# Kernel optimization log

Measured on AMD Instinct MI355X. Metric: run time of the kernel, lower is better.

## Reference

```python
import jax, jax.numpy as jnp
import numpy as np

B, D, MAXC = 16384, 64, 8
NPROB, NCON, TDIM, HID = 50000, 2000, 1024, 256

def setup_inputs() -> dict:
    key = jax.random.key(0)
    ks = jax.random.split(key, 20)
    s = 0.02
    return {
        'prob_ids': jax.random.randint(ks[0], (B,), 0, NPROB),
        'related_concept_index': jax.random.randint(ks[1], (B, MAXC), 0, NCON),
        'filter0': jax.random.randint(ks[2], (B, MAXC), 0, 2),
        'h': jax.random.normal(ks[3], (B, D), jnp.float32),
        'emb': jax.random.normal(ks[4], (B, 2 * D), jnp.float32),
        'operate': jax.random.randint(ks[5], (B, 1), 0, 2).astype(jnp.float32),
        'exercise_text_emb': jax.random.normal(ks[6], (NPROB, TDIM), jnp.float32) * s,
        'concept_text_emb': jax.random.normal(ks[7], (NCON, TDIM), jnp.float32) * s,
        'W1': jax.random.normal(ks[8], (TDIM, HID), jnp.float32) * s,
        'b1': jnp.zeros((HID,), jnp.float32),
        'W2': jax.random.normal(ks[9], (HID, D), jnp.float32) * s,
        'b2': jnp.zeros((D,), jnp.float32),
        'Wp': jax.random.normal(ks[10], (5 * D, 1), jnp.float32) * s,
        'bp': jnp.zeros((1,), jnp.float32),
        'Wx': jax.random.normal(ks[11], (4 * D, 3 * D), jnp.float32) * s,
        'Wh': jax.random.normal(ks[12], (D, 3 * D), jnp.float32) * s,
        'bx': jnp.zeros((3 * D,), jnp.float32),
        'bh': jnp.zeros((3 * D,), jnp.float32),
    }

def reference(prob_ids, related_concept_index, filter0, h, emb, operate,
              exercise_text_emb, concept_text_emb,
              W1, b1, W2, b2, Wp, bp, Wx, Wh, bx, bh):
    def text_proj(x):  # 1024 -> 256 -> 64 (dropout off at inference)
        return jax.nn.relu(x @ W1 + b1) @ W2 + b2

    red_prob = text_proj(exercise_text_emb)      # [NPROB, D]
    red_con = text_proj(concept_text_emb)        # [NCON, D]

    related = red_con[related_concept_index]     # gather: [B, MAXC, D]

    # text weights: cosine similarity of raw BERT embs (torch eps=1e-8)
    q = exercise_text_emb[prob_ids]              # [B, 1024]
    c = concept_text_emb[related_concept_index]  # [B, MAXC, 1024]
    dot = jnp.einsum('bd,bmd->bm', q, c)
    qn = jnp.sqrt(jnp.sum(q * q, axis=-1))[:, None]
    cn = jnp.sqrt(jnp.sum(c * c, axis=-1))
    tw = dot / jnp.maximum(qn * cn, 1e-8)
    tw = jnp.where(filter0 == 0, jnp.float32(-1e9), tw)
    tw = jax.nn.softmax(tw, axis=1)              # [B, MAXC]

    rep = jnp.einsum('bmd,bm->bd', related, tw)  # weighted concept sum
    v = jnp.concatenate([red_prob[prob_ids], rep], axis=1)  # [B, 2D]

    # predictor: funcs(n_layer=1, dim*5, 1) ~ single Linear
    prob = jnp.concatenate([h, v, emb], axis=1) @ Wp + bp   # [B, 1]

    # update_state -> GRU cell (mygru: input 4D, hidden D)
    op = operate
    v_cat = jnp.concatenate([v * op, v * (1 - op)], axis=1)
    e_cat = jnp.concatenate([emb * (1 - op), emb * op], axis=1)
    x = v_cat + e_cat                             # [B, 4D]
    xg = x @ Wx + bx
    hg = h @ Wh + bh
    xr, xz, xn = jnp.split(xg, 3, axis=1)
    hr, hz, hn = jnp.split(hg, 3, axis=1)
    r = jax.nn.sigmoid(xr + hr)
    z = jax.nn.sigmoid(xz + hz)
    n = jnp.tanh(xn + r * hn)
    h_next = (1 - z) * n + z * h                  # [B, D]
    return (prob, h_next)
```

## Files before the change

### kernel.cpp

```cpp
#include <hip/hip_runtime.h>
#include <cstdint>
#include <cstddef>

typedef unsigned short u16;
typedef unsigned char u8;
typedef long long i64;
typedef unsigned long long u64;
typedef __bf16 bf16x8 __attribute__((ext_vector_type(8)));
typedef float f32x4 __attribute__((ext_vector_type(4)));
typedef float f32x2 __attribute__((ext_vector_type(2)));
typedef u16 u16x8 __attribute__((ext_vector_type(8)));

#define B_ 16384
#define D_ 64
#define MAXC_ 8
#define NCON_ 2000
#define NCONP_ 2048
#define TDIM_ 1024
#define HID_ 256

#define VMW(n) asm volatile("s_waitcnt vmcnt(" #n ")" ::: "memory")
#define BAR() __builtin_amdgcn_s_barrier()

__device__ inline u16 f2b(float f){
  unsigned u = __float_as_uint(f);
  u += 0x7fffu + ((u >> 16) & 1u);
  return (u16)(u >> 16);
}
__device__ inline float b2f(u16 u){ return __uint_as_float(((unsigned)u) << 16); }

__device__ inline unsigned pk2fp8(float a, float b){
  return (unsigned)__builtin_amdgcn_cvt_pk_fp8_f32(a, b, 0, false);
}

__device__ inline void gload16(const void* g, void* l){
  __builtin_amdgcn_global_load_lds((const __attribute__((address_space(1))) unsigned*)g,
                                   (__attribute__((address_space(3))) unsigned*)l, 16, 0, 0);
}

__device__ inline float wsum(float v){
  #pragma unroll
  for (int o = 32; o; o >>= 1) v += __shfl_xor(v, o);
  return v;
}
__device__ inline float sigf(float x){ return 1.f / (1.f + __expf(-x)); }

__global__ __launch_bounds__(256) void k_prep(
    const float* __restrict__ ex, const int* __restrict__ pid,
    const float* __restrict__ con,
    const float* __restrict__ W1, const float* __restrict__ W2,
    const float* __restrict__ Wx, const float* __restrict__ Wh,
    const float* __restrict__ bx, const float* __restrict__ bh,
    u8* __restrict__ qb8, float* __restrict__ qn,
    u8* __restrict__ cb8, float* __restrict__ cn,
    u8* __restrict__ W1T8, u16* __restrict__ W2T, u16* __restrict__ WxhT,
    float* __restrict__ bxh)
{
  const int bid = blockIdx.x, tid = threadIdx.x;
  const int lane = tid & 63;
  if (bid < 4096){
    const int b = bid * 4 + (tid >> 6);
    const float* src = ex + (size_t)pid[b] * TDIM_;
    u8* dst8 = qb8 + (size_t)b * TDIM_;
    float ss = 0.f;
    #pragma unroll
    for (int c = 0; c < 4; ++c){
      float4 v = *(const float4*)(src + c * 256 + lane * 4);
      ss += v.x*v.x + v.y*v.y + v.z*v.z + v.w*v.w;
      unsigned lo = pk2fp8(v.x * 32.f, v.y * 32.f);
      unsigned hi = pk2fp8(v.z * 32.f, v.w * 32.f);
      *(unsigned*)(dst8 + c * 256 + lane * 4) = (lo & 0xffffu) | (hi << 16);
    }
    ss = wsum(ss);
    if (lane == 0) qn[b] = sqrtf(ss);
  } else if (bid < 4608){
    const int r = (bid - 4096) * 4 + (tid >> 6);
    u8* dst8 = cb8 + (size_t)r * TDIM_;
    if (r < NCON_){
      const float* src = con + (size_t)r * TDIM_;
      float ss = 0.f;
      #pragma unroll
      for (int c = 0; c < 4; ++c){
        float4 v = *(const float4*)(src + c * 256 + lane * 4);
        ss += v.x*v.x + v.y*v.y + v.z*v.z + v.w*v.w;
        unsigned lo = pk2fp8(v.x * 32.f, v.y * 32.f);
        unsigned hi = pk2fp8(v.z * 32.f, v.w * 32.f);
        *(unsigned*)(dst8 + c * 256 + lane * 4) = (lo & 0xffffu) | (hi << 16);
      }
      ss = wsum(ss);
      if (lane == 0) cn[r] = sqrtf(ss);
    } else {
      #pragma unroll
      for (int c = 0; c < 4; ++c)
        *(unsigned*)(dst8 + c * 256 + lane * 4) = 0u;
    }
  } else {
    int gid = (bid - 4608) * 256 + tid;
    if (gid < 131072){
      int n = gid >> 9, k2 = (gid & 511) * 2;
      unsigned pk = pk2fp8(W1[(size_t)k2 * 256 + n] * 32.f,
                           W1[(size_t)(k2 + 1) * 256 + n] * 32.f);
      *(u16*)(W1T8 + (size_t)n * 1024 + k2) = (u16)pk;
    } else if (gid < 147456){
      int t = gid - 131072;
      int n = t >> 8, k = t & 255;
      W2T[t] = f2b(W2[(size_t)k * 64 + n]);
    } else if (gid < 229376){
      int t = gid - 147456;
      int c = t / 320, k = t % 320;
      int g = (c >> 4) & 3;
      int d = (c >> 6) * 16 + (c & 15);
      float v = 0.f;
      if (k < 256){
        if (g == 0)      v = Wx[(size_t)k * 192 + d];
        else if (g == 1) v = Wx[(size_t)k * 192 + 64 + d];
        else if (g == 2) v = Wx[(size_t)k * 192 + 128 + d];
      } else {
        int kh = k - 256;
        if (g == 0)      v = Wh[(size_t)kh * 192 + d];
        else if (g == 1) v = Wh[(size_t)kh * 192 + 64 + d];
        else if (g == 3) v = Wh[(size_t)kh * 192 + 128 + d];
      }
      WxhT[t] = f2b(v);
    } else if (gid < 229632){
      int c = gid - 229376;
      int g = (c >> 4) & 3;
      int d = (c >> 6) * 16 + (c & 15);
      float v;
      if (g == 0)      v = bx[d] + bh[d];
      else if (g == 1) v = bx[64 + d] + bh[64 + d];
      else if (g == 2) v = bx[128 + d];
      else             v = bh[128 + d];
      bxh[c] = v;
    }
  }
}

__global__ __launch_bounds__(512) void k_mlp(
    const u8* __restrict__ qb8, const u8* __restrict__ cb8,
    const u8* __restrict__ W1T8, const float* __restrict__ b1,
    const u16* __restrict__ W2T, const float* __restrict__ b2,
    float* __restrict__ redq, float* __restrict__ redc)
{
  __shared__ char SMm[53248];
  u16* Hs = (u16*)(SMm + 36864);
  const int tid = threadIdx.x;
  const int lane = tid & 63;
  const int w = tid >> 6;
  const int lr = lane & 15, lq = lane >> 4;
  const bool qside = blockIdx.x < 512;
  const u8* Abase = qside ? qb8 : cb8;
  float* Obase = qside ? redq : redc;
  const int m0 = (qside ? (int)blockIdx.x : ((int)blockIdx.x - 512)) << 5;
  const int rf = w & 1, ch = w >> 1;

  auto stage = [&](int buf, int kt){
    u8* Ab = (u8*)SMm + buf * 18432;
    u8* Bb = Ab + 2048;
    #pragma unroll
    for (int i = 0; i < 2; ++i){
      int e = i * 512 + tid;
      int slot = e >> 2, q4 = e & 3;
      int sw = (slot ^ (slot >> 2)) & 3;
      gload16(W1T8 + (size_t)slot * 1024 + kt * 64 + ((q4 ^ sw) << 4), Bb + e * 16);
    }
    if (tid < 128){
      int slot = tid >> 2, q4 = tid & 3;
      int sw = (slot ^ (slot >> 2)) & 3;
      gload16(Abase + (size_t)(m0 + slot) * TDIM_ + kt * 64 + ((q4 ^ sw) << 4),
              Ab + tid * 16);
    }
  };

  f32x4 acc[4] = {};
  stage(0, 0);
  int buf = 0;
  for (int kt = 0; kt < 16; ++kt){
    if (kt < 15){
      stage(buf ^ 1, kt + 1);
      if (w < 2) VMW(3); else VMW(2);
    } else VMW(0);
    BAR();
    const u8* Ab = (const u8*)SMm + buf * 18432;
    const u8* Bb = Ab + 2048;
    #pragma unroll
    for (int ks = 0; ks < 2; ++ks){
      const int h8 = ks * 4 + lq;
      const int arow = rf * 16 + lr;
      const int asw = (arow ^ (arow >> 2)) & 3;
      i64 a = *(const i64*)(Ab + arow * 64 + (((h8 >> 1) ^ asw) << 4) + (h8 & 1) * 8);
      #pragma unroll
      for (int fc = 0; fc < 4; ++fc){
        int brow = ch * 64 + fc * 16 + lr;
        int bsw = (brow ^ (brow >> 2)) & 3;
        i64 bv = *(const i64*)(Bb + brow * 64 + (((h8 >> 1) ^ bsw) << 4) + (h8 & 1) * 8);
        acc[fc] = __builtin_amdgcn_mfma_f32_16x16x32_fp8_fp8(a, bv, acc[fc], 0, 0, 0);
      }
    }
    BAR();
    buf ^= 1;
  }
  #pragma unroll
  for (int fc = 0; fc < 4; ++fc){
    int col = ch * 64 + fc * 16 + lr;
    float bv = b1[col];
    #pragma unroll
    for (int j = 0; j < 4; ++j){
      int rr = rf * 16 + lq * 4 + j;
      float v = fmaxf(acc[fc][j] * (1.f / 1024.f) + bv, 0.f);
      *(u16*)((char*)Hs + rr * 512 + ((col * 2) ^ ((rr & 7) << 4))) = f2b(v);
    }
  }
  __syncthreads();
  const int rf2 = w & 1, cp = w >> 1;
  f32x4 acc2 = {};
  #pragma unroll
  for (int ks2 = 0; ks2 < 8; ++ks2){
    int rr = rf2 * 16 + lr;
    int kb2 = ks2 * 64 + lq * 16;
    bf16x8 af2 = *(const bf16x8*)((const char*)Hs + rr * 512 + (kb2 ^ ((rr & 7) << 4)));
    bf16x8 w2 = *(const bf16x8*)(W2T + (size_t)(cp * 16 + lr) * 256 + ks2 * 32 + lq * 8);
    acc2 = __builtin_amdgcn_mfma_f32_16x16x32_bf16(af2, w2, acc2, 0, 0, 0);
  }
  {
    int col = cp * 16 + lr;
    float bv = b2[col];
    #pragma unroll
    for (int j = 0; j < 4; ++j){
      int rr = m0 + rf2 * 16 + lq * 4 + j;
      Obase[(size_t)rr * 64 + col] = acc2[j] + bv;
    }
  }
}

__global__ __launch_bounds__(512) void k_mixgru(
    const u8* __restrict__ qb8, const u8* __restrict__ cb8,
    const float* __restrict__ qn, const float* __restrict__ cn,
    const int* __restrict__ rci, const int* __restrict__ filt,
    const float* __restrict__ redq, const float* __restrict__ redc,
    const float* __restrict__ h, const float* __restrict__ emb,
    const float* __restrict__ op, const float* __restrict__ Wp,
    const float* __restrict__ bp, const u16* __restrict__ WxhT,
    const float* __restrict__ bxh, float* __restrict__ prob_out,
    float* __restrict__ outh)
{
  __shared__ char SM[67584];
  u8*    QsF  = (u8*)SM;
  u16*   XH   = (u16*)SM;
  float* DOTS = (float*)(SM + 20480);
  int*   SIDX = (int*)(SM + 32768);
  int*   SFLT = (int*)(SM + 33792);
  u8*    CsB  = (u8*)(SM + 34816);
  u16*   Bs   = (u16*)(SM + 34816);
  const int tid = threadIdx.x;
  const int lane = tid & 63;
  const int w = tid >> 6;
  const int m0 = blockIdx.x << 5;

  auto stageC = [&](int buf, int kt){
    #pragma unroll
    for (int i = 0; i < 2; ++i){
      int e = i * 512 + tid;
      int slot = e >> 2, q4 = e & 3;
      int sw = (slot ^ (slot >> 2)) & 3;
      gload16(cb8 + (size_t)SIDX[slot] * TDIM_ + kt * 64 + ((q4 ^ sw) << 4),
              CsB + buf * 16384 + e * 16);
    }
  };

  if (tid < 256) SIDX[tid] = rci[m0 * MAXC_ + tid];
  else           SFLT[tid - 256] = filt[m0 * MAXC_ + (tid - 256)];
  __syncthreads();
  #pragma unroll
  for (int i = 0; i < 4; ++i){
    int e = i * 512 + tid;
    int row = e >> 6, c16 = e & 63;
    gload16(qb8 + (size_t)(m0 + row) * TDIM_ + ((c16 ^ (row & 7)) << 4),
            QsF + e * 16);
  }
  stageC(0, 0);

  const int R = w >> 2;
  const int cc0 = (w & 3) * 2;
  f32x4 dacc[2] = {};
  int bufc = 0;
  for (int kt = 0; kt < 16; ++kt){
    if (kt < 15){ stageC(bufc ^ 1, kt + 1); VMW(2); }
    else        { VMW(0); }
    BAR();
    const u8* Cs = CsB + bufc * 16384;
    #pragma unroll
    for (int ks = 0; ks < 2; ++ks){
      const int h8 = ks * 4 + (lane >> 4);
      const int arow = R * 16 + (lane & 15);
      const int c16r = kt * 4 + (h8 >> 1);
      i64 a = *(const i64*)(QsF + arow * 1024 + ((c16r ^ (arow & 7)) << 4) + (h8 & 1) * 8);
      #pragma unroll
      for (int t = 0; t < 2; ++t){
        int slot = (R * 8 + cc0 + t) * 16 + (lane & 15);
        int bsw = (slot ^ (slot >> 2)) & 3;
        i64 bfr = *(const i64*)(Cs + slot * 64 + (((h8 >> 1) ^ bsw) << 4) + (h8 & 1) * 8);
        dacc[t] = __builtin_amdgcn_mfma_f32_16x16x32_fp8_fp8(a, bfr, dacc[t], 0, 0, 0);
      }
    }
    BAR();
    bufc ^= 1;
  }
  #pragma unroll
  for (int t = 0; t < 2; ++t){
    const int cc = cc0 + t;
    const int col = lane & 15;
    #pragma unroll
    for (int j = 0; j < 4; ++j){
      int tr = (lane >> 4) * 4 + j;
      if (tr == 2 * cc && col < 8)       DOTS[(R * 16 + tr) * 8 + col] = dacc[t][j];
      if (tr == 2 * cc + 1 && col >= 8)  DOTS[(R * 16 + tr) * 8 + col - 8] = dacc[t][j];
    }
  }
  auto stageB = [&](int kt){
    #pragma unroll
    for (int i = 0; i < 4; ++i){
      int cc = i * 512 + tid;
      int r2 = cc >> 3, s2 = cc & 7;
      gload16(WxhT + (size_t)r2 * 320 + kt * 64 + ((s2 ^ (r2 & 7)) << 3), &Bs[cc * 8]);
    }
  };
  __syncthreads();
  stageB(0);

  for (int i = 0; i < 4; ++i){
    const int r = w * 4 + i;
    const int b = m0 + r;
    int idxm[MAXC_];
    #pragma unroll
    for (int m = 0; m < MAXC_; ++m) idxm[m] = SIDX[r * MAXC_ + m];
    const float qnb = qn[b];
    float sv[MAXC_]; float mx = -3.0e38f;
    #pragma unroll
    for (int m = 0; m < MAXC_; ++m){
      float dnm = fmaxf(qnb * cn[idxm[m]], 1e-8f);
      float s = (SFLT[r * MAXC_ + m] == 0) ? -1e9f
              : DOTS[r * 8 + m] * (1.f / 1024.f) / dnm;
      sv[m] = s; mx = fmaxf(mx, s);
    }
    float se = 0.f;
    #pragma unroll
    for (int m = 0; m < MAXC_; ++m){ sv[m] = __expf(sv[m] - mx); se += sv[m]; }
    const float inv = 1.f / se;
    float rep = 0.f;
    #pragma unroll
    for (int m = 0; m < MAXC_; ++m) rep += sv[m] * redc[(size_t)idxm[m] * D_ + lane];
    rep *= inv;
    const float v0 = redq[(size_t)b * D_ + lane];
    const float hv = h[(size_t)b * D_ + lane];
    const float e0 = emb[(size_t)b * 128 + lane];
    const float e1 = emb[(size_t)b * 128 + 64 + lane];
    float p = hv * Wp[lane] + v0 * Wp[64 + lane] + rep * Wp[128 + lane]
            + e0 * Wp[192 + lane] + e1 * Wp[256 + lane];
    p = wsum(p);
    if (lane == 0) prob_out[b] = p + bp[0];
    const float o = op[b], om = 1.f - o;
    auto xst = [&](int col, float v){
      *(u16*)((char*)XH + r * 640 + ((col * 2) ^ ((r & 7) << 4))) = f2b(v);
    };
    xst(lane,        v0 * o  + e0 * om);
    xst(64 + lane,   rep * o + e1 * om);
    xst(128 + lane,  v0 * om + e0 * o);
    xst(192 + lane,  rep * om + e1 * o);
    xst(256 + lane,  hv);
  }
  __syncthreads();

  const int lr = lane & 15, lq = lane >> 4;
  const int rh = w & 1, cc2 = w >> 1;
  f32x4 acc[4] = {};
  for (int kt = 0; kt < 5; ++kt){
    VMW(0);
    BAR();
    #pragma unroll
    for (int ks = 0; ks < 2; ++ks){
      const int kb = ks * 64 + lq * 16;
      int rra = rh * 16 + lr;
      bf16x8 af = *(const bf16x8*)((const char*)XH + rra * 640 +
                                   ((kt * 128 + kb) ^ ((rra & 7) << 4)));
      bf16x8 bfr[4];
      #pragma unroll
      for (int fc = 0; fc < 4; ++fc){
        int rr = cc2 * 64 + fc * 16 + lr;
        bfr[fc] = *(const bf16x8*)((const char*)Bs + rr * 128 + (kb ^ ((rr & 7) << 4)));
      }
      #pragma unroll
      for (int fc = 0; fc < 4; ++fc)
        acc[fc] = __builtin_amdgcn_mfma_f32_16x16x32_bf16(af, bfr[fc], acc[fc], 0, 0, 0);
    }
    BAR();
    if (kt < 4) stageB(kt + 1);
  }
  const int d = cc2 * 16 + lr;
  float bg[4];
  #pragma unroll
  for (int g = 0; g < 4; ++g) bg[g] = bxh[cc2 * 64 + g * 16 + lr];
  #pragma unroll
  for (int j = 0; j < 4; ++j){
    float rv = sigf(acc[0][j] + bg[0]);
    float zv = sigf(acc[1][j] + bg[1]);
    float nv = tanhf(acc[2][j] + bg[2] + rv * (acc[3][j] + bg[3]));
    int rr = m0 + rh * 16 + lq * 4 + j;
    float hv = h[(size_t)rr * 64 + d];
    outh[(size_t)rr * 64 + d] = (1.f - zv) * nv + zv * hv;
  }
}

extern "C" void kernel_launch(void* const* d_in, const int* in_sizes, int n_in,
                              void* d_out, int out_size, void* d_ws, size_t ws_size,
                              hipStream_t stream) {
  const int*   prob_ids = (const int*)  d_in[0];
  const int*   rci      = (const int*)  d_in[1];
  const int*   filt     = (const int*)  d_in[2];
  const float* h        = (const float*)d_in[3];
  const float* emb      = (const float*)d_in[4];
  const float* op       = (const float*)d_in[5];
  const float* ex       = (const float*)d_in[6];
  const float* con      = (const float*)d_in[7];
  const float* W1       = (const float*)d_in[8];
  const float* b1       = (const float*)d_in[9];
  const float* W2       = (const float*)d_in[10];
  const float* b2       = (const float*)d_in[11];
  const float* Wp       = (const float*)d_in[12];
  const float* bp       = (const float*)d_in[13];
  const float* Wx       = (const float*)d_in[14];
  const float* Wh       = (const float*)d_in[15];
  const float* bx       = (const float*)d_in[16];
  const float* bh       = (const float*)d_in[17];
  float* out = (float*)d_out;

  char* w = (char*)d_ws;
  size_t off = 0;
  auto alloc = [&](size_t bytes){ size_t o = off; off = (off + bytes + 255) & ~(size_t)255; return o; };
  u8*    qb8  = (u8*)   (w + alloc((size_t)B_ * TDIM_));
  u8*    cb8  = (u8*)   (w + alloc((size_t)NCONP_ * TDIM_));
  float* qn   = (float*)(w + alloc((size_t)B_ * 4));
  float* cn   = (float*)(w + alloc((size_t)NCONP_ * 4));
  float* redq = (float*)(w + alloc((size_t)B_ * D_ * 4));
  float* redc = (float*)(w + alloc((size_t)NCONP_ * D_ * 4));
  u8*    W1T8 = (u8*)   (w + alloc((size_t)HID_ * TDIM_));
  u16*   W2T  = (u16*)  (w + alloc((size_t)D_ * HID_ * 2));
  u16*   WxhT = (u16*)  (w + alloc((size_t)256 * 320 * 2));
  float* bxh  = (float*)(w + alloc((size_t)256 * 4));

  k_prep<<<5505, 256, 0, stream>>>(ex, prob_ids, con, W1, W2, Wx, Wh, bx, bh,
                                   qb8, qn, cb8, cn, W1T8, W2T, WxhT, bxh);
  k_mlp<<<576, 512, 0, stream>>>(qb8, cb8, W1T8, b1, W2T, b2, redq, redc);
  k_mixgru<<<512, 512, 0, stream>>>(qb8, cb8, qn, cn, rci, filt, redq, redc,
                                    h, emb, op, Wp, bp, WxhT, bxh, out, out + B_);
}
```

Before: 71.45 us.

## Load concept fp8 fragments directly to registers instead of LDS double-buffering

In the mixgru kernel, the cosine-dot phase no longer stages gathered concept fp8 rows through double-buffered LDS with barriers. Each lane now loads its MFMA B fragments straight from global memory into registers, prefetching one k-tile ahead, which removes the per-iteration barriers and the LDS traffic. Launch bounds also request 4 waves per SIMD. The trade is uncoalesced 8-byte global gathers in place of 16-byte async LDS loads, plus tighter register limits.

```diff
diff --git a/kernel.cpp b/kernel.cpp
--- a/kernel.cpp
+++ b/kernel.cpp
@@ -8,7 +8,6 @@
 typedef unsigned long long u64;
 typedef __bf16 bf16x8 __attribute__((ext_vector_type(8)));
 typedef float f32x4 __attribute__((ext_vector_type(4)));
-typedef float f32x2 __attribute__((ext_vector_type(2)));
 typedef u16 u16x8 __attribute__((ext_vector_type(8)));
 
 #define B_ 16384
@@ -27,7 +26,6 @@
   u += 0x7fffu + ((u >> 16) & 1u);
   return (u16)(u >> 16);
 }
-__device__ inline float b2f(u16 u){ return __uint_as_float(((unsigned)u) << 16); }
 
 __device__ inline unsigned pk2fp8(float a, float b){
   return (unsigned)__builtin_amdgcn_cvt_pk_fp8_f32(a, b, 0, false);
@@ -233,7 +231,7 @@
   }
 }
 
-__global__ __launch_bounds__(512) void k_mixgru(
+__global__ __launch_bounds__(512, 4) void k_mixgru(
     const u8* __restrict__ qb8, const u8* __restrict__ cb8,
     const float* __restrict__ qn, const float* __restrict__ cn,
     const int* __restrict__ rci, const int* __restrict__ filt,
@@ -250,27 +248,13 @@
   float* DOTS = (float*)(SM + 20480);
   int*   SIDX = (int*)(SM + 32768);
   int*   SFLT = (int*)(SM + 33792);
-  u8*    CsB  = (u8*)(SM + 34816);
   u16*   Bs   = (u16*)(SM + 34816);
   const int tid = threadIdx.x;
   const int lane = tid & 63;
   const int w = tid >> 6;
+  const int lr = lane & 15, lq = lane >> 4;
   const int m0 = blockIdx.x << 5;
 
-  auto stageC = [&](int buf, int kt){
-    #pragma unroll
-    for (int i = 0; i < 2; ++i){
-      int e = i * 512 + tid;
-      int slot = e >> 2, q4 = e & 3;
-      int sw = (slot ^ (slot >> 2)) & 3;
-      gload16(cb8 + (size_t)SIDX[slot] * TDIM_ + kt * 64 + ((q4 ^ sw) << 4),
-              CsB + buf * 16384 + e * 16);
-    }
-  };
-
-  if (tid < 256) SIDX[tid] = rci[m0 * MAXC_ + tid];
-  else           SFLT[tid - 256] = filt[m0 * MAXC_ + (tid - 256)];
-  __syncthreads();
   #pragma unroll
   for (int i = 0; i < 4; ++i){
     int e = i * 512 + tid;
@@ -278,41 +262,48 @@
     gload16(qb8 + (size_t)(m0 + row) * TDIM_ + ((c16 ^ (row & 7)) << 4),
             QsF + e * 16);
   }
-  stageC(0, 0);
+  if (tid < 256) SIDX[tid] = rci[m0 * MAXC_ + tid];
+  else           SFLT[tid - 256] = filt[m0 * MAXC_ + (tid - 256)];
+  __syncthreads();
 
   const int R = w >> 2;
   const int cc0 = (w & 3) * 2;
+  const u8* brow0 = cb8 + (size_t)SIDX[(R * 8 + cc0) * 16 + lr] * TDIM_ + lq * 8;
+  const u8* brow1 = cb8 + (size_t)SIDX[(R * 8 + cc0 + 1) * 16 + lr] * TDIM_ + lq * 8;
   f32x4 dacc[2] = {};
-  int bufc = 0;
+  u64 c00 = *(const u64*)(brow0);
+  u64 c01 = *(const u64*)(brow0 + 32);
+  u64 c10 = *(const u64*)(brow1);
+  u64 c11 = *(const u64*)(brow1 + 32);
   for (int kt = 0; kt < 16; ++kt){
-    if (kt < 15){ stageC(bufc ^ 1, kt + 1); VMW(2); }
-    else        { VMW(0); }
-    BAR();
-    const u8* Cs = CsB + bufc * 16384;
+    u64 n00, n01, n10, n11;
+    if (kt < 15){
+      n00 = *(const u64*)(brow0 + (kt + 1) * 64);
+      n01 = *(const u64*)(brow0 + (kt + 1) * 64 + 32);
+      n10 = *(const u64*)(brow1 + (kt + 1) * 64);
+      n11 = *(const u64*)(brow1 + (kt + 1) * 64 + 32);
+    }
     #pragma unroll
     for (int ks = 0; ks < 2; ++ks){
-      const int h8 = ks * 4 + (lane >> 4);
-      const int arow = R * 16 + (lane & 15);
+      const int h8 = ks * 4 + lq;
+      const int arow = R * 16 + lr;
       const int c16r = kt * 4 + (h8 >> 1);
       i64 a = *(const i64*)(QsF + arow * 1024 + ((c16r ^ (arow & 7)) << 4) + (h8 & 1) * 8);
-      #pragma unroll
-      for (int t = 0; t < 2; ++t){
-        int slot = (R * 8 + cc0 + t) * 16 + (lane & 15);
-        int bsw = (slot ^ (slot >> 2)) & 3;
-        i64 bfr = *(const i64*)(Cs + slot * 64 + (((h8 >> 1) ^ bsw) << 4) + (h8 & 1) * 8);
-        dacc[t] = __builtin_amdgcn_mfma_f32_16x16x32_fp8_fp8(a, bfr, dacc[t], 0, 0, 0);
-      }
-    }
-    BAR();
-    bufc ^= 1;
-  }
+      dacc[0] = __builtin_amdgcn_mfma_f32_16x16x32_fp8_fp8(a, (i64)(ks ? c01 : c00),
+                                                           dacc[0], 0, 0, 0);
+      dacc[1] = __builtin_amdgcn_mfma_f32_16x16x32_fp8_fp8(a, (i64)(ks ? c11 : c10),
+                                                           dacc[1], 0, 0, 0);
+    }
+    c00 = n00; c01 = n01; c10 = n10; c11 = n11;
+  }
+  __syncthreads();
   #pragma unroll
   for (int t = 0; t < 2; ++t){
     const int cc = cc0 + t;
     const int col = lane & 15;
     #pragma unroll
     for (int j = 0; j < 4; ++j){
-      int tr = (lane >> 4) * 4 + j;
+      int tr = lq * 4 + j;
       if (tr == 2 * cc && col < 8)       DOTS[(R * 16 + tr) * 8 + col] = dacc[t][j];
       if (tr == 2 * cc + 1 && col >= 8)  DOTS[(R * 16 + tr) * 8 + col - 8] = dacc[t][j];
     }
@@ -371,7 +362,6 @@
   }
   __syncthreads();
 
-  const int lr = lane & 15, lq = lane >> 4;
   const int rh = w & 1, cc2 = w >> 1;
   f32x4 acc[4] = {};
   for (int kt = 0; kt < 5; ++kt){
```

New measurement: 89.62 us. 25.4% more time.
